# Kernel tuning notes

Hardware: AMD Instinct MI355X
Metric: run time of the kernel (lower is better)

The kernel has to match this reference:

```python
import jax, jax.numpy as jnp
import numpy as np

DIM = 192
HEADS = 6
WIN = 64  # 8*8
EPS = 1e-12


def setup_inputs() -> dict:
    key = jax.random.key(0)
    ks = jax.random.split(key, 10)
    s = 0.02
    return {
        "qx": jax.random.normal(ks[0], (8192, WIN, DIM), jnp.float32),
        "kvx": jax.random.normal(ks[1], (4096, WIN, DIM), jnp.float32),
        "pos": jax.random.normal(ks[2], (1, WIN, DIM), jnp.float32) * s,
        "Wq": jax.random.normal(ks[3], (DIM, DIM), jnp.float32) * s,
        "bq": jnp.zeros((DIM,), jnp.float32),
        "Wkv": jax.random.normal(ks[4], (2 * DIM, DIM), jnp.float32) * s,
        "bkv": jnp.zeros((2 * DIM,), jnp.float32),
        "Wp": jax.random.normal(ks[5], (DIM, DIM), jnp.float32) * s,
        "bp": jnp.zeros((DIM,), jnp.float32),
    }


def _l2norm(x):
    # F.normalize: x / max(||x||_2, eps) along last dim
    n = jnp.sqrt(jnp.sum(x * x, axis=-1, keepdims=True))
    return x / jnp.maximum(n, EPS)


def reference(qx, kvx, pos, Wq, bq, Wkv, bkv, Wp, bp):
    B_q, q_len, C = qx.shape
    B_kv, kv_len, _ = kvx.shape
    tile_num = B_q // B_kv
    kvx = jnp.tile(kvx, (tile_num, 1, 1))
    qx = qx + pos
    q = qx @ Wq.T + bq                       # [Bq, q, C]
    kv = kvx @ Wkv.T + bkv                   # [Bq, kv, 2C]
    k, v = kv[..., :C], kv[..., C:]
    hd = C // HEADS
    q = q.reshape(B_q, q_len, HEADS, hd).transpose(0, 2, 1, 3)
    k = k.reshape(B_q, kv_len, HEADS, hd).transpose(0, 2, 1, 3)
    v = v.reshape(B_q, kv_len, HEADS, hd).transpose(0, 2, 1, 3)
    scale = 1.0 / np.sqrt(C).astype(np.float32)
    attn = jnp.einsum("bhqd,bhkd->bhqk", _l2norm(q), _l2norm(k)) * scale
    attn = jax.nn.softmax(attn, axis=-1)
    x = jnp.einsum("bhqk,bhkd->bhqd", attn, v)
    x = x.transpose(0, 2, 1, 3).reshape(B_q, q_len, C)
    return x @ Wp.T + bp
```

## Files before the change

### kernel.cpp

```cpp
#include <hip/hip_runtime.h>
#include <hip/hip_bf16.h>

#define TPB   512
#define CDIM  192
#define LDA   200
#define LDK   200
#define LDVT  72
#define LDST  200
#define VTOFF 12800
#define SCALE 0.07216878364870323f
#define EPSF  1e-12f

using short8 = __attribute__((ext_vector_type(8))) short;
using f32x4  = __attribute__((ext_vector_type(4))) float;
using us4    = __attribute__((ext_vector_type(4))) unsigned short;

__device__ __forceinline__ unsigned short hc(float f) {
  __hip_bfloat16 h = __float2bfloat16(f);
  unsigned short u; __builtin_memcpy(&u, &h, 2); return u;
}
__device__ __forceinline__ unsigned pack2(float x, float y) {
  return (unsigned)hc(x) | ((unsigned)hc(y) << 16);
}
__device__ __forceinline__ uint2 packa(f32x4 a) {
  return make_uint2(pack2(a[0], a[1]), pack2(a[2], a[3]));
}
#define MFMA(a, b, c) __builtin_amdgcn_mfma_f32_16x16x32_bf16((a), (b), (c), 0, 0, 0)
#define SCHED_FENCE() __builtin_amdgcn_sched_barrier(0)

#define NWQ  36864
#define NWKV 73728
#define NWP  36864
__global__ void cvt_weights(const float* __restrict__ Wq, const float* __restrict__ Wkv,
                            const float* __restrict__ Wp, unsigned short* __restrict__ o) {
  int i = blockIdx.x * blockDim.x + threadIdx.x;
  if (i < NWQ) o[i] = hc(Wq[i]);
  else if (i < NWQ + NWKV) o[i] = hc(Wkv[i - NWQ]);
  else if (i < NWQ + NWKV + NWP) o[i] = hc(Wp[i - NWQ - NWKV]);
}

__global__ __launch_bounds__(TPB, 4) void wa_v12(
    const float* __restrict__ qx, const float* __restrict__ kvx,
    const float* __restrict__ pos,
    const float* __restrict__ bq, const float* __restrict__ bkv,
    const float* __restrict__ bp,
    const unsigned short* __restrict__ Wqb, const unsigned short* __restrict__ Wkvb,
    const unsigned short* __restrict__ Wpb,
    float* __restrict__ out, int BQ, int BKV)
{
  __shared__ __align__(16) unsigned short sA[64 * LDA];
  __shared__ __align__(16) unsigned short sU[26624];

  const int tid = threadIdx.x;
  const int wid = tid >> 6;
  const int l15 = (tid & 63) & 15;
  const int l4  = (tid & 63) >> 4;

  int g = blockIdx.x;
  int w;
  if (BQ == 2 * BKV && (BKV & 7) == 0) {
    w = ((g >> 4) << 3) + (g & 7) + (((g >> 3) & 1) ? BKV : 0);
  } else {
    w = g;
  }
  const size_t qoff  = (size_t)w * (64 * CDIM);
  const size_t kvoff = (size_t)(w % BKV) * (64 * CDIM);

  const int srcA = l15 + 32 * (l4 & 1);
  const int srcB = srcA + 16;
  const int sel  = l4 >> 1;
  auto redistC = [&](f32x4 cA, f32x4 cB) -> short8 {
    unsigned iA0 = pack2(cA[0], cA[1]), iA1 = pack2(cA[2], cA[3]);
    unsigned iB0 = pack2(cB[0], cB[1]), iB1 = pack2(cB[2], cB[3]);
    unsigned A00 = (unsigned)__shfl((int)iA0, srcA);
    unsigned A01 = (unsigned)__shfl((int)iA1, srcA);
    unsigned A10 = (unsigned)__shfl((int)iB0, srcA);
    unsigned A11 = (unsigned)__shfl((int)iB1, srcA);
    unsigned B00 = (unsigned)__shfl((int)iA0, srcB);
    unsigned B01 = (unsigned)__shfl((int)iA1, srcB);
    unsigned B10 = (unsigned)__shfl((int)iB0, srcB);
    unsigned B11 = (unsigned)__shfl((int)iB1, srcB);
    union { uint4 u; short8 s; } uu;
    uu.u.x = sel ? A10 : A00;
    uu.u.y = sel ? A11 : A01;
    uu.u.z = sel ? B10 : B00;
    uu.u.w = sel ? B11 : B01;
    return uu.s;
  };

  {
    const float4* gq = (const float4*)(qx + qoff);
    const float4* p4 = (const float4*)pos;
    #pragma unroll
    for (int t = 0; t < 6; ++t) {
      int e = tid + t * TPB, row = e / 48, c4 = e % 48;
      float4 a = gq[e], p = p4[e];
      us4 wq;
      wq.x = hc(a.x + p.x); wq.y = hc(a.y + p.y); wq.z = hc(a.z + p.z); wq.w = hc(a.w + p.w);
      *(us4*)&sA[row * LDA + c4 * 4] = wq;
    }
    const float4* gk = (const float4*)(kvx + kvoff);
    #pragma unroll
    for (int t = 0; t < 6; ++t) {
      int e = tid + t * TPB, row = e / 48, c4 = e % 48;
      float4 k = gk[e];
      us4 wk; wk.x = hc(k.x); wk.y = hc(k.y); wk.z = hc(k.z); wk.w = hc(k.w);
      *(us4*)&sU[row * LDST + c4 * 4] = wk;
    }
  }
  __syncthreads();

  auto kproj = [&](int h, short8* kres) {
    f32x4 kacc[4][2];
    #pragma unroll
    for (int mh = 0; mh < 2; ++mh) {
      float4 bk = *(const float4*)&bkv[32 * h + 16 * mh + 4 * l4];
      #pragma unroll
      for (int n = 0; n < 4; ++n) kacc[n][mh] = f32x4{bk.x, bk.y, bk.z, bk.w};
    }
    #pragma unroll
    for (int ks = 0; ks < 6; ++ks) {
      short8 act[4];
      #pragma unroll
      for (int n = 0; n < 4; ++n)
        act[n] = *(const short8*)&sU[(16 * n + l15) * LDST + ks * 32 + 8 * l4];
      #pragma unroll
      for (int mh = 0; mh < 2; ++mh) {
        short8 kw = *(const short8*)&Wkvb[(size_t)(32 * h + 16 * mh + l15) * CDIM + ks * 32 + 8 * l4];
        #pragma unroll
        for (int n = 0; n < 4; ++n) kacc[n][mh] = MFMA(kw, act[n], kacc[n][mh]);
      }
    }
    #pragma unroll
    for (int n = 0; n < 4; ++n) {
      float ss = 0.f;
      #pragma unroll
      for (int mh = 0; mh < 2; ++mh)
        #pragma unroll
        for (int r = 0; r < 4; ++r) ss += kacc[n][mh][r] * kacc[n][mh][r];
      ss += __shfl_xor(ss, 16);
      ss += __shfl_xor(ss, 32);
      float sc = 1.0f / fmaxf(sqrtf(ss), EPSF);
      #pragma unroll
      for (int mh = 0; mh < 2; ++mh)
        #pragma unroll
        for (int r = 0; r < 4; ++r) kacc[n][mh][r] *= sc;
      kres[n] = redistC(kacc[n][0], kacc[n][1]);
    }
  };
  auto vproj = [&](int h) {
    f32x4 vacc[4][2];
    #pragma unroll
    for (int nv = 0; nv < 2; ++nv) {
      float bv = bkv[CDIM + 32 * h + 16 * nv + l15];
      #pragma unroll
      for (int m = 0; m < 4; ++m) vacc[m][nv] = f32x4{bv, bv, bv, bv};
    }
    #pragma unroll
    for (int ks = 0; ks < 6; ++ks) {
      short8 act[4];
      #pragma unroll
      for (int n = 0; n < 4; ++n)
        act[n] = *(const short8*)&sU[(16 * n + l15) * LDST + ks * 32 + 8 * l4];
      #pragma unroll
      for (int nv = 0; nv < 2; ++nv) {
        short8 vw = *(const short8*)&Wkvb[(size_t)(CDIM + 32 * h + 16 * nv + l15) * CDIM + ks * 32 + 8 * l4];
        #pragma unroll
        for (int m = 0; m < 4; ++m) vacc[m][nv] = MFMA(act[m], vw, vacc[m][nv]);
      }
    }
    #pragma unroll
    for (int m = 0; m < 4; ++m)
      #pragma unroll
      for (int nv = 0; nv < 2; ++nv)
        *(uint2*)&sU[VTOFF + (32 * h + 16 * nv + l15) * LDVT + 16 * m + 4 * l4] = packa(vacc[m][nv]);
  };
  auto qproj = [&](int h, short8* qres) {
    f32x4 qacc[4][2];
    #pragma unroll
    for (int mh = 0; mh < 2; ++mh) {
      float4 bk = *(const float4*)&bq[32 * h + 16 * mh + 4 * l4];
      #pragma unroll
      for (int n = 0; n < 4; ++n) qacc[n][mh] = f32x4{bk.x, bk.y, bk.z, bk.w};
    }
    #pragma unroll
    for (int ks = 0; ks < 6; ++ks) {
      short8 act[4];
      #pragma unroll
      for (int n = 0; n < 4; ++n)
        act[n] = *(const short8*)&sA[(16 * n + l15) * LDA + ks * 32 + 8 * l4];
      #pragma unroll
      for (int mh = 0; mh < 2; ++mh) {
        short8 qw = *(const short8*)&Wqb[(size_t)(32 * h + 16 * mh + l15) * CDIM + ks * 32 + 8 * l4];
        #pragma unroll
        for (int n = 0; n < 4; ++n) qacc[n][mh] = MFMA(qw, act[n], qacc[n][mh]);
      }
    }
    #pragma unroll
    for (int n = 0; n < 4; ++n) {
      float ss = 0.f;
      #pragma unroll
      for (int mh = 0; mh < 2; ++mh)
        #pragma unroll
        for (int r = 0; r < 4; ++r) ss += qacc[n][mh][r] * qacc[n][mh][r];
      ss += __shfl_xor(ss, 16);
      ss += __shfl_xor(ss, 32);
      float sc = SCALE / fmaxf(sqrtf(ss), EPSF);
      #pragma unroll
      for (int mh = 0; mh < 2; ++mh)
        #pragma unroll
        for (int r = 0; r < 4; ++r) qacc[n][mh][r] *= sc;
      qres[n] = redistC(qacc[n][0], qacc[n][1]);
    }
  };

  short8 kres[4];
  const bool hasK = (wid < 6);
  if (hasK) kproj(wid, kres);
  else      vproj(wid - 6);
  SCHED_FENCE();
  if (wid < 4) vproj(wid + 2);
  __syncthreads();

  if (hasK) {
    #pragma unroll
    for (int n = 0; n < 4; ++n)
      *(short8*)&sU[(16 * n + l15) * LDK + wid * 32 + 8 * l4] = kres[n];
  }
  SCHED_FENCE();
  short8 qres[4];
  if (wid < 6) qproj(wid, qres);
  __syncthreads();

  if (wid < 6) {
    #pragma unroll
    for (int n = 0; n < 4; ++n)
      *(short8*)&sA[(16 * n + l15) * LDA + wid * 32 + 8 * l4] = qres[n];
  }
  __syncthreads();

  {
    const int t  = wid & 3;
    const int h0 = 3 * (wid >> 2);
    #pragma unroll
    for (int i = 0; i < 3; ++i) {
      const int hh = h0 + i;
      short8 qb = *(const short8*)&sA[(16 * t + l15) * LDA + hh * 32 + 8 * l4];
      f32x4 c[4];
      #pragma unroll
      for (int n = 0; n < 4; ++n) {
        short8 ak = *(const short8*)&sU[(16 * n + l15) * LDK + hh * 32 + 8 * l4];
        f32x4 z = f32x4{0.f, 0.f, 0.f, 0.f};
        c[n] = MFMA(ak, qb, z);
      }
      float mx = c[0][0];
      #pragma unroll
      for (int n = 0; n < 4; ++n)
        #pragma unroll
        for (int r = 0; r < 4; ++r) mx = fmaxf(mx, c[n][r]);
      mx = fmaxf(mx, __shfl_xor(mx, 16));
      mx = fmaxf(mx, __shfl_xor(mx, 32));
      float sum = 0.f;
      #pragma unroll
      for (int n = 0; n < 4; ++n)
        #pragma unroll
        for (int r = 0; r < 4; ++r) { c[n][r] = __expf(c[n][r] - mx); sum += c[n][r]; }
      sum += __shfl_xor(sum, 16);
      sum += __shfl_xor(sum, 32);
      const float inv = 1.0f / sum;
      #pragma unroll
      for (int n = 0; n < 4; ++n)
        #pragma unroll
        for (int r = 0; r < 4; ++r) c[n][r] *= inv;
      short8 pa0 = redistC(c[0], c[1]);
      short8 pa1 = redistC(c[2], c[3]);
      f32x4 cx0 = f32x4{0.f, 0.f, 0.f, 0.f};
      f32x4 cx1 = f32x4{0.f, 0.f, 0.f, 0.f};
      {
        short8 av00 = *(const short8*)&sU[VTOFF + (hh * 32 + l15) * LDVT + 8 * l4];
        short8 av01 = *(const short8*)&sU[VTOFF + (hh * 32 + l15) * LDVT + 32 + 8 * l4];
        cx0 = MFMA(av00, pa0, cx0);
        cx0 = MFMA(av01, pa1, cx0);
        short8 av10 = *(const short8*)&sU[VTOFF + (hh * 32 + 16 + l15) * LDVT + 8 * l4];
        short8 av11 = *(const short8*)&sU[VTOFF + (hh * 32 + 16 + l15) * LDVT + 32 + 8 * l4];
        cx1 = MFMA(av10, pa0, cx1);
        cx1 = MFMA(av11, pa1, cx1);
      }
      short8 xf = redistC(cx0, cx1);
      *(short8*)&sA[(16 * t + l15) * LDA + hh * 32 + 8 * l4] = xf;
    }
  }
  __syncthreads();

  {
    {
      const int n = wid;
      f32x4 oacc[4];
      float bv = bp[n * 16 + l15];
      #pragma unroll
      for (int m = 0; m < 4; ++m) oacc[m] = f32x4{bv, bv, bv, bv};
      #pragma unroll
      for (int ks = 0; ks < 6; ++ks) {
        short8 pw = *(const short8*)&Wpb[(size_t)(n * 16 + l15) * CDIM + ks * 32 + 8 * l4];
        #pragma unroll
        for (int m = 0; m < 4; ++m) {
          short8 xa = *(const short8*)&sA[(16 * m + l15) * LDA + ks * 32 + 8 * l4];
          oacc[m] = MFMA(xa, pw, oacc[m]);
        }
      }
      #pragma unroll
      for (int m = 0; m < 4; ++m)
        #pragma unroll
        for (int r = 0; r < 4; ++r)
          out[qoff + (size_t)(16 * m + 4 * l4 + r) * CDIM + n * 16 + l15] = oacc[m][r];
    }
    SCHED_FENCE();
    if (wid < 4) {
      const int n = wid + 8;
      f32x4 oacc[4];
      float bv = bp[n * 16 + l15];
      #pragma unroll
      for (int m = 0; m < 4; ++m) oacc[m] = f32x4{bv, bv, bv, bv};
      #pragma unroll
      for (int ks = 0; ks < 6; ++ks) {
        short8 pw = *(const short8*)&Wpb[(size_t)(n * 16 + l15) * CDIM + ks * 32 + 8 * l4];
        #pragma unroll
        for (int m = 0; m < 4; ++m) {
          short8 xa = *(const short8*)&sA[(16 * m + l15) * LDA + ks * 32 + 8 * l4];
          oacc[m] = MFMA(xa, pw, oacc[m]);
        }
      }
      #pragma unroll
      for (int m = 0; m < 4; ++m)
        #pragma unroll
        for (int r = 0; r < 4; ++r)
          out[qoff + (size_t)(16 * m + 4 * l4 + r) * CDIM + n * 16 + l15] = oacc[m][r];
    }
  }
}

extern "C" void kernel_launch(void* const* d_in, const int* in_sizes, int n_in,
                              void* d_out, int out_size, void* d_ws, size_t ws_size,
                              hipStream_t stream) {
  const float* qx  = (const float*)d_in[0];
  const float* kvx = (const float*)d_in[1];
  const float* pos = (const float*)d_in[2];
  const float* Wq  = (const float*)d_in[3];
  const float* bq  = (const float*)d_in[4];
  const float* Wkv = (const float*)d_in[5];
  const float* bkv = (const float*)d_in[6];
  const float* Wp  = (const float*)d_in[7];
  const float* bp  = (const float*)d_in[8];
  float* out = (float*)d_out;
  unsigned short* wsb = (unsigned short*)d_ws;

  const int BQ  = in_sizes[0] / (64 * CDIM);
  const int BKV = in_sizes[1] / (64 * CDIM);

  const int ncvt = NWQ + NWKV + NWP;
  cvt_weights<<<(ncvt + 255) / 256, 256, 0, stream>>>(Wq, Wkv, Wp, wsb);

  wa_v12<<<BQ, TPB, 0, stream>>>(qx, kvx, pos, bq, bkv, bp,
                                 wsb, wsb + NWQ, wsb + NWQ + NWKV, out, BQ, BKV);
}
```

Measured before the change: 474.7 us.

## Keep per-head K, V, Q in registers and drop LDS staging

Each of the first six waves now computes K, V and Q for one head and holds them in MFMA operand registers, so attention runs directly from registers with no LDS round-trips for K, V^T or Q. The shared buffer shrinks from about 26.6K to 12.8K shorts, which may allow more resident blocks, and the attention output is written into sU for the output projection. In exchange, waves 6-7 now sit idle through the projection and attention phases, so the work is less balanced across the block, and register pressure rises.

```diff
diff --git a/kernel.cpp b/kernel.cpp
--- a/kernel.cpp
+++ b/kernel.cpp
@@ -4,10 +4,7 @@
 #define TPB   512
 #define CDIM  192
 #define LDA   200
-#define LDK   200
-#define LDVT  72
 #define LDST  200
-#define VTOFF 12800
 #define SCALE 0.07216878364870323f
 #define EPSF  1e-12f
 
@@ -21,9 +18,6 @@
 }
 __device__ __forceinline__ unsigned pack2(float x, float y) {
   return (unsigned)hc(x) | ((unsigned)hc(y) << 16);
-}
-__device__ __forceinline__ uint2 packa(f32x4 a) {
-  return make_uint2(pack2(a[0], a[1]), pack2(a[2], a[3]));
 }
 #define MFMA(a, b, c) __builtin_amdgcn_mfma_f32_16x16x32_bf16((a), (b), (c), 0, 0, 0)
 #define SCHED_FENCE() __builtin_amdgcn_sched_barrier(0)
@@ -39,7 +33,7 @@
   else if (i < NWQ + NWKV + NWP) o[i] = hc(Wp[i - NWQ - NWKV]);
 }
 
-__global__ __launch_bounds__(TPB, 4) void wa_v12(
+__global__ __launch_bounds__(TPB, 4) void wa_v13(
     const float* __restrict__ qx, const float* __restrict__ kvx,
     const float* __restrict__ pos,
     const float* __restrict__ bq, const float* __restrict__ bkv,
@@ -49,7 +43,7 @@
     float* __restrict__ out, int BQ, int BKV)
 {
   __shared__ __align__(16) unsigned short sA[64 * LDA];
-  __shared__ __align__(16) unsigned short sU[26624];
+  __shared__ __align__(16) unsigned short sU[64 * LDST];
 
   const int tid = threadIdx.x;
   const int wid = tid >> 6;
@@ -110,148 +104,128 @@
   }
   __syncthreads();
 
-  auto kproj = [&](int h, short8* kres) {
-    f32x4 kacc[4][2];
+  const int h = wid;
+
+  short8 kres[4];
+  short8 av[2][2];
+  if (wid < 6) {
+    {
+      f32x4 kacc[4][2];
+      #pragma unroll
+      for (int mh = 0; mh < 2; ++mh) {
+        float4 bk = *(const float4*)&bkv[32 * h + 16 * mh + 4 * l4];
+        #pragma unroll
+        for (int n = 0; n < 4; ++n) kacc[n][mh] = f32x4{bk.x, bk.y, bk.z, bk.w};
+      }
+      #pragma unroll
+      for (int ks = 0; ks < 6; ++ks) {
+        short8 act[4];
+        #pragma unroll
+        for (int n = 0; n < 4; ++n)
+          act[n] = *(const short8*)&sU[(16 * n + l15) * LDST + ks * 32 + 8 * l4];
+        #pragma unroll
+        for (int mh = 0; mh < 2; ++mh) {
+          short8 kw = *(const short8*)&Wkvb[(size_t)(32 * h + 16 * mh + l15) * CDIM + ks * 32 + 8 * l4];
+          #pragma unroll
+          for (int n = 0; n < 4; ++n) kacc[n][mh] = MFMA(kw, act[n], kacc[n][mh]);
+        }
+      }
+      #pragma unroll
+      for (int n = 0; n < 4; ++n) {
+        float ss = 0.f;
+        #pragma unroll
+        for (int mh = 0; mh < 2; ++mh)
+          #pragma unroll
+          for (int r = 0; r < 4; ++r) ss += kacc[n][mh][r] * kacc[n][mh][r];
+        ss += __shfl_xor(ss, 16);
+        ss += __shfl_xor(ss, 32);
+        float sc = 1.0f / fmaxf(sqrtf(ss), EPSF);
+        #pragma unroll
+        for (int mh = 0; mh < 2; ++mh)
+          #pragma unroll
+          for (int r = 0; r < 4; ++r) kacc[n][mh][r] *= sc;
+        kres[n] = redistC(kacc[n][0], kacc[n][1]);
+      }
+    }
+    SCHED_FENCE();
+    {
+      f32x4 vacc[4][2];
+      #pragma unroll
+      for (int nv = 0; nv < 2; ++nv) {
+        float bv = bkv[CDIM + 32 * h + 16 * nv + l15];
+        #pragma unroll
+        for (int m = 0; m < 4; ++m) vacc[m][nv] = f32x4{bv, bv, bv, bv};
+      }
+      #pragma unroll
+      for (int ks = 0; ks < 6; ++ks) {
+        short8 act[4];
+        #pragma unroll
+        for (int n = 0; n < 4; ++n)
+          act[n] = *(const short8*)&sU[(16 * n + l15) * LDST + ks * 32 + 8 * l4];
+        #pragma unroll
+        for (int nv = 0; nv < 2; ++nv) {
+          short8 vw = *(const short8*)&Wkvb[(size_t)(CDIM + 32 * h + 16 * nv + l15) * CDIM + ks * 32 + 8 * l4];
+          #pragma unroll
+          for (int m = 0; m < 4; ++m) vacc[m][nv] = MFMA(act[m], vw, vacc[m][nv]);
+        }
+      }
+      #pragma unroll
+      for (int cc = 0; cc < 2; ++cc)
+        #pragma unroll
+        for (int nv = 0; nv < 2; ++nv)
+          av[cc][nv] = redistC(vacc[2 * cc][nv], vacc[2 * cc + 1][nv]);
+    }
+  }
+  __syncthreads();
+
+  if (wid < 6) {
+    short8 qres[4];
+    {
+      f32x4 qacc[4][2];
+      #pragma unroll
+      for (int mh = 0; mh < 2; ++mh) {
+        float4 bk = *(const float4*)&bq[32 * h + 16 * mh + 4 * l4];
+        #pragma unroll
+        for (int n = 0; n < 4; ++n) qacc[n][mh] = f32x4{bk.x, bk.y, bk.z, bk.w};
+      }
+      #pragma unroll
+      for (int ks = 0; ks < 6; ++ks) {
+        short8 act[4];
+        #pragma unroll
+        for (int n = 0; n < 4; ++n)
+          act[n] = *(const short8*)&sA[(16 * n + l15) * LDA + ks * 32 + 8 * l4];
+        #pragma unroll
+        for (int mh = 0; mh < 2; ++mh) {
+          short8 qw = *(const short8*)&Wqb[(size_t)(32 * h + 16 * mh + l15) * CDIM + ks * 32 + 8 * l4];
+          #pragma unroll
+          for (int n = 0; n < 4; ++n) qacc[n][mh] = MFMA(qw, act[n], qacc[n][mh]);
+        }
+      }
+      #pragma unroll
+      for (int n = 0; n < 4; ++n) {
+        float ss = 0.f;
+        #pragma unroll
+        for (int mh = 0; mh < 2; ++mh)
+          #pragma unroll
+          for (int r = 0; r < 4; ++r) ss += qacc[n][mh][r] * qacc[n][mh][r];
+        ss += __shfl_xor(ss, 16);
+        ss += __shfl_xor(ss, 32);
+        float sc = SCALE / fmaxf(sqrtf(ss), EPSF);
+        #pragma unroll
+        for (int mh = 0; mh < 2; ++mh)
+          #pragma unroll
+          for (int r = 0; r < 4; ++r) qacc[n][mh][r] *= sc;
+        qres[n] = redistC(qacc[n][0], qacc[n][1]);
+      }
+    }
+    SCHED_FENCE();
     #pragma unroll
-    for (int mh = 0; mh < 2; ++mh) {
-      float4 bk = *(const float4*)&bkv[32 * h + 16 * mh + 4 * l4];
-      #pragma unroll
-      for (int n = 0; n < 4; ++n) kacc[n][mh] = f32x4{bk.x, bk.y, bk.z, bk.w};
-    }
-    #pragma unroll
-    for (int ks = 0; ks < 6; ++ks) {
-      short8 act[4];
-      #pragma unroll
-      for (int n = 0; n < 4; ++n)
-        act[n] = *(const short8*)&sU[(16 * n + l15) * LDST + ks * 32 + 8 * l4];
-      #pragma unroll
-      for (int mh = 0; mh < 2; ++mh) {
-        short8 kw = *(const short8*)&Wkvb[(size_t)(32 * h + 16 * mh + l15) * CDIM + ks * 32 + 8 * l4];
-        #pragma unroll
-        for (int n = 0; n < 4; ++n) kacc[n][mh] = MFMA(kw, act[n], kacc[n][mh]);
-      }
-    }
-    #pragma unroll
-    for (int n = 0; n < 4; ++n) {
-      float ss = 0.f;
-      #pragma unroll
-      for (int mh = 0; mh < 2; ++mh)
-        #pragma unroll
-        for (int r = 0; r < 4; ++r) ss += kacc[n][mh][r] * kacc[n][mh][r];
-      ss += __shfl_xor(ss, 16);
-      ss += __shfl_xor(ss, 32);
-      float sc = 1.0f / fmaxf(sqrtf(ss), EPSF);
-      #pragma unroll
-      for (int mh = 0; mh < 2; ++mh)
-        #pragma unroll
-        for (int r = 0; r < 4; ++r) kacc[n][mh][r] *= sc;
-      kres[n] = redistC(kacc[n][0], kacc[n][1]);
-    }
-  };
-  auto vproj = [&](int h) {
-    f32x4 vacc[4][2];
-    #pragma unroll
-    for (int nv = 0; nv < 2; ++nv) {
-      float bv = bkv[CDIM + 32 * h + 16 * nv + l15];
-      #pragma unroll
-      for (int m = 0; m < 4; ++m) vacc[m][nv] = f32x4{bv, bv, bv, bv};
-    }
-    #pragma unroll
-    for (int ks = 0; ks < 6; ++ks) {
-      short8 act[4];
-      #pragma unroll
-      for (int n = 0; n < 4; ++n)
-        act[n] = *(const short8*)&sU[(16 * n + l15) * LDST + ks * 32 + 8 * l4];
-      #pragma unroll
-      for (int nv = 0; nv < 2; ++nv) {
-        short8 vw = *(const short8*)&Wkvb[(size_t)(CDIM + 32 * h + 16 * nv + l15) * CDIM + ks * 32 + 8 * l4];
-        #pragma unroll
-        for (int m = 0; m < 4; ++m) vacc[m][nv] = MFMA(act[m], vw, vacc[m][nv]);
-      }
-    }
-    #pragma unroll
-    for (int m = 0; m < 4; ++m)
-      #pragma unroll
-      for (int nv = 0; nv < 2; ++nv)
-        *(uint2*)&sU[VTOFF + (32 * h + 16 * nv + l15) * LDVT + 16 * m + 4 * l4] = packa(vacc[m][nv]);
-  };
-  auto qproj = [&](int h, short8* qres) {
-    f32x4 qacc[4][2];
-    #pragma unroll
-    for (int mh = 0; mh < 2; ++mh) {
-      float4 bk = *(const float4*)&bq[32 * h + 16 * mh + 4 * l4];
-      #pragma unroll
-      for (int n = 0; n < 4; ++n) qacc[n][mh] = f32x4{bk.x, bk.y, bk.z, bk.w};
-    }
-    #pragma unroll
-    for (int ks = 0; ks < 6; ++ks) {
-      short8 act[4];
-      #pragma unroll
-      for (int n = 0; n < 4; ++n)
-        act[n] = *(const short8*)&sA[(16 * n + l15) * LDA + ks * 32 + 8 * l4];
-      #pragma unroll
-      for (int mh = 0; mh < 2; ++mh) {
-        short8 qw = *(const short8*)&Wqb[(size_t)(32 * h + 16 * mh + l15) * CDIM + ks * 32 + 8 * l4];
-        #pragma unroll
-        for (int n = 0; n < 4; ++n) qacc[n][mh] = MFMA(qw, act[n], qacc[n][mh]);
-      }
-    }
-    #pragma unroll
-    for (int n = 0; n < 4; ++n) {
-      float ss = 0.f;
-      #pragma unroll
-      for (int mh = 0; mh < 2; ++mh)
-        #pragma unroll
-        for (int r = 0; r < 4; ++r) ss += qacc[n][mh][r] * qacc[n][mh][r];
-      ss += __shfl_xor(ss, 16);
-      ss += __shfl_xor(ss, 32);
-      float sc = SCALE / fmaxf(sqrtf(ss), EPSF);
-      #pragma unroll
-      for (int mh = 0; mh < 2; ++mh)
-        #pragma unroll
-        for (int r = 0; r < 4; ++r) qacc[n][mh][r] *= sc;
-      qres[n] = redistC(qacc[n][0], qacc[n][1]);
-    }
-  };
-
-  short8 kres[4];
-  const bool hasK = (wid < 6);
-  if (hasK) kproj(wid, kres);
-  else      vproj(wid - 6);
-  SCHED_FENCE();
-  if (wid < 4) vproj(wid + 2);
-  __syncthreads();
-
-  if (hasK) {
-    #pragma unroll
-    for (int n = 0; n < 4; ++n)
-      *(short8*)&sU[(16 * n + l15) * LDK + wid * 32 + 8 * l4] = kres[n];
-  }
-  SCHED_FENCE();
-  short8 qres[4];
-  if (wid < 6) qproj(wid, qres);
-  __syncthreads();
-
-  if (wid < 6) {
-    #pragma unroll
-    for (int n = 0; n < 4; ++n)
-      *(short8*)&sA[(16 * n + l15) * LDA + wid * 32 + 8 * l4] = qres[n];
-  }
-  __syncthreads();
-
-  {
-    const int t  = wid & 3;
-    const int h0 = 3 * (wid >> 2);
-    #pragma unroll
-    for (int i = 0; i < 3; ++i) {
-      const int hh = h0 + i;
-      short8 qb = *(const short8*)&sA[(16 * t + l15) * LDA + hh * 32 + 8 * l4];
+    for (int t = 0; t < 4; ++t) {
       f32x4 c[4];
       #pragma unroll
       for (int n = 0; n < 4; ++n) {
-        short8 ak = *(const short8*)&sU[(16 * n + l15) * LDK + hh * 32 + 8 * l4];
         f32x4 z = f32x4{0.f, 0.f, 0.f, 0.f};
-        c[n] = MFMA(ak, qb, z);
+        c[n] = MFMA(kres[n], qres[t], z);
       }
       float mx = c[0][0];
       #pragma unroll
@@ -276,18 +250,12 @@
       short8 pa1 = redistC(c[2], c[3]);
       f32x4 cx0 = f32x4{0.f, 0.f, 0.f, 0.f};
       f32x4 cx1 = f32x4{0.f, 0.f, 0.f, 0.f};
-      {
-        short8 av00 = *(const short8*)&sU[VTOFF + (hh * 32 + l15) * LDVT + 8 * l4];
-        short8 av01 = *(const short8*)&sU[VTOFF + (hh * 32 + l15) * LDVT + 32 + 8 * l4];
-        cx0 = MFMA(av00, pa0, cx0);
-        cx0 = MFMA(av01, pa1, cx0);
-        short8 av10 = *(const short8*)&sU[VTOFF + (hh * 32 + 16 + l15) * LDVT + 8 * l4];
-        short8 av11 = *(const short8*)&sU[VTOFF + (hh * 32 + 16 + l15) * LDVT + 32 + 8 * l4];
-        cx1 = MFMA(av10, pa0, cx1);
-        cx1 = MFMA(av11, pa1, cx1);
-      }
+      cx0 = MFMA(av[0][0], pa0, cx0);
+      cx0 = MFMA(av[1][0], pa1, cx0);
+      cx1 = MFMA(av[0][1], pa0, cx1);
+      cx1 = MFMA(av[1][1], pa1, cx1);
       short8 xf = redistC(cx0, cx1);
-      *(short8*)&sA[(16 * t + l15) * LDA + hh * 32 + 8 * l4] = xf;
+      *(short8*)&sU[(16 * t + l15) * LDST + h * 32 + 8 * l4] = xf;
     }
   }
   __syncthreads();
@@ -304,7 +272,7 @@
         short8 pw = *(const short8*)&Wpb[(size_t)(n * 16 + l15) * CDIM + ks * 32 + 8 * l4];
         #pragma unroll
         for (int m = 0; m < 4; ++m) {
-          short8 xa = *(const short8*)&sA[(16 * m + l15) * LDA + ks * 32 + 8 * l4];
+          short8 xa = *(const short8*)&sU[(16 * m + l15) * LDST + ks * 32 + 8 * l4];
           oacc[m] = MFMA(xa, pw, oacc[m]);
         }
       }
@@ -315,8 +283,8 @@
           out[qoff + (size_t)(16 * m + 4 * l4 + r) * CDIM + n * 16 + l15] = oacc[m][r];
     }
     SCHED_FENCE();
-    if (wid < 4) {
-      const int n = wid + 8;
+    if (wid >= 4) {
+      const int n = wid + 4;
       f32x4 oacc[4];
       float bv = bp[n * 16 + l15];
       #pragma unroll
@@ -326,7 +294,7 @@
         short8 pw = *(const short8*)&Wpb[(size_t)(n * 16 + l15) * CDIM + ks * 32 + 8 * l4];
         #pragma unroll
         for (int m = 0; m < 4; ++m) {
-          short8 xa = *(const short8*)&sA[(16 * m + l15) * LDA + ks * 32 + 8 * l4];
+          short8 xa = *(const short8*)&sU[(16 * m + l15) * LDST + ks * 32 + 8 * l4];
           oacc[m] = MFMA(xa, pw, oacc[m]);
         }
       }
@@ -360,6 +328,6 @@
   const int ncvt = NWQ + NWKV + NWP;
   cvt_weights<<<(ncvt + 255) / 256, 256, 0, stream>>>(Wq, Wkv, Wp, wsb);
 
-  wa_v12<<<BQ, TPB, 0, stream>>>(qx, kvx, pos, bq, bkv, bp,
+  wa_v13<<<BQ, TPB, 0, stream>>>(qx, kvx, pos, bq, bkv, bp,
                                  wsb, wsb + NWQ, wsb + NWQ + NWKV, out, BQ, BKV);
 }
```

Result: no change. 482.4 us (+1.6%).
